# Kernel optimization log

Measured on AMD Instinct MI355X. Metric: run time of the kernel, lower is better.

## Reference

```python
import math
import jax, jax.numpy as jnp
import numpy as np

B, S, D = 8, 1024, 1024
H, DK = 16, 64
NUM_BUCKETS, MAX_DIST = 32, 128


def _relative_position_bucket(relative_position, num_buckets=NUM_BUCKETS, max_distance=MAX_DIST):
    # bidirectional=True branch of T5's bucket fn
    nb = num_buckets // 2
    n = -relative_position
    ret = (n < 0).astype(jnp.int32) * nb
    n = jnp.abs(n)
    max_exact = nb // 2
    is_small = n < max_exact
    n_safe = jnp.maximum(n, 1).astype(jnp.float32)
    val_if_large = max_exact + (
        jnp.log(n_safe / max_exact) / math.log(max_distance / max_exact) * (nb - max_exact)
    ).astype(jnp.int32)
    val_if_large = jnp.minimum(val_if_large, nb - 1)
    return ret + jnp.where(is_small, n, val_if_large)


def compute_bias(rel_emb, qlen, klen):
    ctx = jnp.arange(qlen)[:, None]
    mem = jnp.arange(klen)[None, :]
    rp_bucket = _relative_position_bucket(mem - ctx)          # [q, k]
    values = rel_emb[rp_bucket]                                # [q, k, H]
    return jnp.transpose(values, (2, 0, 1))[None]              # [1, H, q, k]


def setup_inputs() -> dict:
    key = jax.random.key(0)
    ks = jax.random.split(key, 6)
    sc = 0.02
    return {
        "x": jax.random.normal(ks[0], (B, S, D), jnp.float32),
        "Wq": jax.random.normal(ks[1], (D, H * DK), jnp.float32) * sc,
        "Wk": jax.random.normal(ks[2], (D, H * DK), jnp.float32) * sc,
        "Wv": jax.random.normal(ks[3], (D, H * DK), jnp.float32) * sc,
        "Wo": jax.random.normal(ks[4], (H * DK, D), jnp.float32) * sc,
        "rel_emb": jax.random.normal(ks[5], (NUM_BUCKETS, H), jnp.float32),
    }


def reference(x, Wq, Wk, Wv, Wo, rel_emb):
    bs, qlen, _ = x.shape

    def shape(t):  # [B, S, H*DK] -> [B, H, S, DK]
        return t.reshape(bs, -1, H, DK).transpose(0, 2, 1, 3)

    q = shape(x @ Wq)
    k = shape(x @ Wk)
    v = shape(x @ Wv)
    # T5 attention: NO 1/sqrt(dk) scaling
    scores = jnp.einsum("bhqd,bhkd->bhqk", q, k)
    position_bias = compute_bias(rel_emb, qlen, qlen)
    scores = scores + position_bias
    weights = jax.nn.softmax(scores.astype(jnp.float32), axis=-1).astype(scores.dtype)
    context = jnp.einsum("bhqk,bhkd->bhqd", weights, v)
    context = context.transpose(0, 2, 1, 3).reshape(bs, qlen, H * DK)
    return context @ Wo
```

## Files before the change

kernel.cpp:

```cpp
#include <hip/hip_runtime.h>
#include <stdint.h>

typedef uint16_t u16;
typedef uint32_t u32;
typedef __bf16 bf16;
typedef bf16 bf16x8 __attribute__((ext_vector_type(8)));
typedef bf16 bf16x4 __attribute__((ext_vector_type(4)));
typedef float f32x4 __attribute__((ext_vector_type(4)));
typedef u16 u16x4 __attribute__((ext_vector_type(4)));

#define MFMA(a, b, c) __builtin_amdgcn_mfma_f32_16x16x32_bf16((a), (b), (c), 0, 0, 0)

#define BATCH 8
#define SEQ 1024
#define DMODEL 1024
#define NH 16
#define DK 64
#define LOG2E 1.4426950408889634f

__device__ __forceinline__ u16 bfbits(float f) {
    bf16 h = (bf16)f;
    return __builtin_bit_cast(u16, h);
}

__device__ __forceinline__ float exp2_raw(float x) {
    float r;
    asm("v_exp_f32 %0, %1" : "=v"(r) : "v"(x));
    return r;
}

__device__ __forceinline__ void gload_lds16(const u16* g, u16* l) {
    __builtin_amdgcn_global_load_lds(
        (__attribute__((address_space(1))) void*)g,
        (__attribute__((address_space(3))) void*)l, 16, 0, 0);
}

__global__ __launch_bounds__(256) void prep_kernel(
        const float* __restrict__ x, const float* __restrict__ W0,
        const float* __restrict__ W1, const float* __restrict__ W2,
        const float* __restrict__ W3, const float* __restrict__ rel_emb,
        u16* __restrict__ xb, u16* __restrict__ T0, u16* __restrict__ T1,
        u16* __restrict__ T2, u16* __restrict__ T3, f32x4* __restrict__ F4) {
    __shared__ u16 Ts[64 * 72];
    const int bid = blockIdx.x, tid = threadIdx.x;
    if (bid < 8192) {
        size_t id = (size_t)bid * 256 + tid;
        f32x4 v = *(const f32x4*)(x + id * 4);
        bf16x4 o;
        o[0] = (bf16)v[0]; o[1] = (bf16)v[1]; o[2] = (bf16)v[2]; o[3] = (bf16)v[3];
        *(bf16x4*)(xb + id * 4) = o;
    } else if (bid < 9216) {
        const int t = bid - 8192;
        const int z = t >> 8, rem = t & 255;
        const float* W = (z == 0) ? W0 : (z == 1) ? W1 : (z == 2) ? W2 : W3;
        u16* T = (z == 0) ? T0 : (z == 1) ? T1 : (z == 2) ? T2 : T3;
        const int k0 = (rem >> 4) * 64, n0 = (rem & 15) * 64;
        const int r16 = tid >> 4, c0 = (tid & 15) * 4;
        #pragma unroll
        for (int rr = 0; rr < 4; rr++) {
            int r = rr * 16 + r16;
            f32x4 vv = *(const f32x4*)&W[(size_t)(k0 + r) * 1024 + n0 + c0];
            #pragma unroll
            for (int i = 0; i < 4; i++) Ts[(c0 + i) * 72 + r] = bfbits(vv[i]);
        }
        __syncthreads();
        int n = tid >> 2, seg = (tid & 3) * 16;
        *(bf16x8*)&T[(size_t)(n0 + n) * 1024 + k0 + seg] = *(const bf16x8*)&Ts[n * 72 + seg];
        *(bf16x8*)&T[(size_t)(n0 + n) * 1024 + k0 + seg + 8] =
            *(const bf16x8*)&Ts[n * 72 + seg + 8];
    } else {
        int id = (bid - 9216) * 256 + tid;
        if (id >= NH * 2047) return;
        int h = id / 2047, tt0 = id % 2047;
        f32x4 o;
        #pragma unroll
        for (int j = 0; j < 4; j++) {
            int tt = tt0 + j;
            float val = 0.f;
            if (tt <= 2046) {
                int rel = tt - 1023;
                int n = -rel;
                int b = 0;
                if (n < 0) { b = 16; n = -n; }
                int v;
                if (n < 8) {
                    v = n;
                } else {
                    int e = 31 - __clz(n);
                    int f = 2 * e + ((unsigned)(n * n) >= (1u << (2 * e + 1)) ? 1 : 0);
                    v = min(2 + f, 15);
                }
                val = LOG2E * rel_emb[(b + v) * NH + h];
            }
            o[j] = val;
        }
        F4[(size_t)h * 2047 + tt0] = o;
    }
}

__global__ __launch_bounds__(256) void gemm_qkv_kernel(
        const u16* __restrict__ xb,
        const u16* __restrict__ Wqt, const u16* __restrict__ Wkt, const u16* __restrict__ Wvt,
        u16* __restrict__ qb, u16* __restrict__ kb, u16* __restrict__ vb) {
    __shared__ u16 As[8192];
    __shared__ u16 Bs[8192];
    const int z = blockIdx.y >> 3;
    const u16* Bt = (z == 0) ? Wqt : (z == 1) ? Wkt : Wvt;
    const int m0 = blockIdx.x * 128, n0 = (blockIdx.y & 7) * 128;
    const int tid = threadIdx.x, w = tid >> 6, lane = tid & 63;
    const int quad = lane >> 4, l16 = lane & 15;
    const int rw = w >> 1, cw = w & 1;
    const int srow = lane >> 2, sseg = lane & 3;

    f32x4 acc[4][4];
    #pragma unroll
    for (int i = 0; i < 4; i++)
        #pragma unroll
        for (int j = 0; j < 4; j++) acc[i][j] = (f32x4){0.f, 0.f, 0.f, 0.f};

    for (int kk = 0; kk < 1024; kk += 64) {
        __syncthreads();
        #pragma unroll
        for (int p = 0; p < 2; p++) {
            #pragma unroll
            for (int r = 0; r < 2; r++) {
                int base = r * 64 + w * 16;
                int row = base + srow;
                gload_lds16(&xb[(size_t)(m0 + row) * 1024 + kk + p * 32 + sseg * 8],
                            &As[p * 4096 + base * 32]);
                gload_lds16(&Bt[(size_t)(n0 + row) * 1024 + kk + p * 32 + sseg * 8],
                            &Bs[p * 4096 + base * 32]);
            }
        }
        __syncthreads();
        #pragma unroll
        for (int p = 0; p < 2; p++) {
            bf16x8 af[4], bfr[4];
            #pragma unroll
            for (int mt = 0; mt < 4; mt++)
                af[mt] = *(const bf16x8*)&As[p * 4096 + (rw * 64 + mt * 16 + l16) * 32 + quad * 8];
            #pragma unroll
            for (int nt = 0; nt < 4; nt++)
                bfr[nt] = *(const bf16x8*)&Bs[p * 4096 + (cw * 64 + nt * 16 + l16) * 32 + quad * 8];
            #pragma unroll
            for (int mt = 0; mt < 4; mt++)
                #pragma unroll
                for (int nt = 0; nt < 4; nt++)
                    acc[mt][nt] = MFMA(af[mt], bfr[nt], acc[mt][nt]);
        }
    }

    #pragma unroll
    for (int mt = 0; mt < 4; mt++) {
        int gmBase = m0 + rw * 64 + mt * 16 + quad * 4;
        #pragma unroll
        for (int nt = 0; nt < 4; nt++) {
            int gn = n0 + cw * 64 + nt * 16 + l16;
            int h = gn >> 6, dk = gn & 63;
            if (z == 2) {
                int b_ = gmBase >> 10, s0 = gmBase & 1023;
                u16x4 pk = { bfbits(acc[mt][nt][0]), bfbits(acc[mt][nt][1]),
                             bfbits(acc[mt][nt][2]), bfbits(acc[mt][nt][3]) };
                *(u16x4*)&vb[(((size_t)b_ * NH + h) * DK + dk) * SEQ + s0] = pk;
            } else {
                u16* o = z ? kb : qb;
                #pragma unroll
                for (int r = 0; r < 4; r++) {
                    int gm = gmBase + r;
                    int b_ = gm >> 10, s = gm & 1023;
                    float sv = acc[mt][nt][r];
                    if (z == 0) sv *= LOG2E;
                    o[(((size_t)b_ * NH + h) * SEQ + s) * DK + dk] = bfbits(sv);
                }
            }
        }
    }
}

__global__ __launch_bounds__(256) void gemm_out_kernel(
        const u16* __restrict__ ctx, const u16* __restrict__ Wot, float* __restrict__ out) {
    __shared__ u16 As[8192];
    __shared__ u16 Bs[8192];
    const int m0 = blockIdx.x * 128, n0 = blockIdx.y * 128;
    const int tid = threadIdx.x, w = tid >> 6, lane = tid & 63;
    const int quad = lane >> 4, l16 = lane & 15;
    const int rw = w >> 1, cw = w & 1;
    const int srow = lane >> 2, sseg = lane & 3;

    f32x4 acc[4][4];
    #pragma unroll
    for (int i = 0; i < 4; i++)
        #pragma unroll
        for (int j = 0; j < 4; j++) acc[i][j] = (f32x4){0.f, 0.f, 0.f, 0.f};

    for (int kk = 0; kk < 1024; kk += 64) {
        __syncthreads();
        #pragma unroll
        for (int p = 0; p < 2; p++) {
            #pragma unroll
            for (int r = 0; r < 2; r++) {
                int base = r * 64 + w * 16;
                int row = base + srow;
                gload_lds16(&ctx[(size_t)(m0 + row) * 1024 + kk + p * 32 + sseg * 8],
                            &As[p * 4096 + base * 32]);
                gload_lds16(&Wot[(size_t)(n0 + row) * 1024 + kk + p * 32 + sseg * 8],
                            &Bs[p * 4096 + base * 32]);
            }
        }
        __syncthreads();
        #pragma unroll
        for (int p = 0; p < 2; p++) {
            bf16x8 af[4], bfr[4];
            #pragma unroll
            for (int mt = 0; mt < 4; mt++)
                af[mt] = *(const bf16x8*)&As[p * 4096 + (rw * 64 + mt * 16 + l16) * 32 + quad * 8];
            #pragma unroll
            for (int nt = 0; nt < 4; nt++)
                bfr[nt] = *(const bf16x8*)&Bs[p * 4096 + (cw * 64 + nt * 16 + l16) * 32 + quad * 8];
            #pragma unroll
            for (int mt = 0; mt < 4; mt++)
                #pragma unroll
                for (int nt = 0; nt < 4; nt++)
                    acc[mt][nt] = MFMA(af[mt], bfr[nt], acc[mt][nt]);
        }
    }

    #pragma unroll
    for (int mt = 0; mt < 4; mt++) {
        int gmBase = m0 + rw * 64 + mt * 16 + quad * 4;
        #pragma unroll
        for (int nt = 0; nt < 4; nt++) {
            int gn = n0 + cw * 64 + nt * 16 + l16;
            #pragma unroll
            for (int r = 0; r < 4; r++)
                out[(size_t)(gmBase + r) * 1024 + gn] = acc[mt][nt][r];
        }
    }
}

__global__ __launch_bounds__(256) void attn_kernel(
        const u16* __restrict__ qb, const u16* __restrict__ kb,
        const u16* __restrict__ vb, const f32x4* __restrict__ F4,
        u16* __restrict__ ctx) {
    __shared__ u16 Kt[64 * 72];
    __shared__ u16 Vt[64 * 72];
    __shared__ u16 Pt[4][32 * 40];
    const int bh = blockIdx.x;
    const int h = bh & (NH - 1), b_ = bh >> 4;
    const int tid = threadIdx.x, w = tid >> 6, lane = tid & 63;
    const int quad = lane >> 4, l16 = lane & 15;
    const int q0 = blockIdx.y * 128 + w * 32;

    const f32x4* F4h = F4 + (size_t)h * 2047;

    bf16x8 bq[2][2];
    #pragma unroll
    for (int mt = 0; mt < 2; mt++) {
        const u16* qrow = qb + ((size_t)bh * SEQ + q0 + mt * 16 + l16) * DK;
        bq[mt][0] = *(const bf16x8*)(qrow + quad * 8);
        bq[mt][1] = *(const bf16x8*)(qrow + 32 + quad * 8);
    }

    float l_[2] = {0.f, 0.f};
    f32x4 oacc[2][4];
    #pragma unroll
    for (int mt = 0; mt < 2; mt++)
        #pragma unroll
        for (int dt = 0; dt < 4; dt++) oacc[mt][dt] = (f32x4){0.f, 0.f, 0.f, 0.f};

    const int srow = tid >> 3, sseg = tid & 7;

    const u16* kbase_p = kb + (size_t)bh * SEQ * DK;
    const u16* vbase_p = vb + (size_t)bh * DK * SEQ;

    bf16x8 kr0 = *(const bf16x8*)&kbase_p[(size_t)srow * DK + sseg * 8];
    bf16x8 kr1 = *(const bf16x8*)&kbase_p[(size_t)(srow + 32) * DK + sseg * 8];
    bf16x8 vr0 = *(const bf16x8*)&vbase_p[(size_t)srow * SEQ + sseg * 8];
    bf16x8 vr1 = *(const bf16x8*)&vbase_p[(size_t)(srow + 32) * SEQ + sseg * 8];

    for (int kt = 0; kt < 16; kt++) {
        const int kbase = kt * 64;
        __syncthreads();
        *(bf16x8*)&Kt[srow * 72 + sseg * 8] = kr0;
        *(bf16x8*)&Kt[(srow + 32) * 72 + sseg * 8] = kr1;
        *(bf16x8*)&Vt[srow * 72 + sseg * 8] = vr0;
        *(bf16x8*)&Vt[(srow + 32) * 72 + sseg * 8] = vr1;
        if (kt < 15) {
            const int nb = kbase + 64;
            kr0 = *(const bf16x8*)&kbase_p[(size_t)(nb + srow) * DK + sseg * 8];
            kr1 = *(const bf16x8*)&kbase_p[(size_t)(nb + srow + 32) * DK + sseg * 8];
            vr0 = *(const bf16x8*)&vbase_p[(size_t)srow * SEQ + nb + sseg * 8];
            vr1 = *(const bf16x8*)&vbase_p[(size_t)(srow + 32) * SEQ + nb + sseg * 8];
        }
        __syncthreads();

        f32x4 sc[2][4];
        #pragma unroll
        for (int mt = 0; mt < 2; mt++)
            #pragma unroll
            for (int nt = 0; nt < 4; nt++) {
                int t0 = (kbase + nt * 16 + quad * 4) - (q0 + mt * 16 + l16) + 1023;
                sc[mt][nt] = F4h[t0];
            }
        #pragma unroll
        for (int nt = 0; nt < 4; nt++) {
            bf16x8 ak0 = *(const bf16x8*)&Kt[(nt * 16 + l16) * 72 + quad * 8];
            bf16x8 ak1 = *(const bf16x8*)&Kt[(nt * 16 + l16) * 72 + 32 + quad * 8];
            #pragma unroll
            for (int mt = 0; mt < 2; mt++) {
                sc[mt][nt] = MFMA(ak0, bq[mt][0], sc[mt][nt]);
                sc[mt][nt] = MFMA(ak1, bq[mt][1], sc[mt][nt]);
            }
        }

        #pragma unroll
        for (int c = 0; c < 2; c++) {
            #pragma unroll
            for (int mt = 0; mt < 2; mt++) {
                #pragma unroll
                for (int i = 0; i < 2; i++) {
                    int nt = 2 * c + i;
                    float p0 = exp2_raw(sc[mt][nt][0]);
                    float p1 = exp2_raw(sc[mt][nt][1]);
                    float p2 = exp2_raw(sc[mt][nt][2]);
                    float p3 = exp2_raw(sc[mt][nt][3]);
                    l_[mt] += (p0 + p1) + (p2 + p3);
                    bf16x4 pk;
                    pk[0] = (bf16)p0; pk[1] = (bf16)p1;
                    pk[2] = (bf16)p2; pk[3] = (bf16)p3;
                    *(bf16x4*)&Pt[w][(mt * 16 + l16) * 40 + i * 16 + quad * 4] = pk;
                }
            }
            bf16x8 bp[2];
            #pragma unroll
            for (int mt = 0; mt < 2; mt++)
                bp[mt] = *(const bf16x8*)&Pt[w][(mt * 16 + l16) * 40 + quad * 8];
            #pragma unroll
            for (int dt = 0; dt < 4; dt++) {
                bf16x8 av = *(const bf16x8*)&Vt[(dt * 16 + l16) * 72 + c * 32 + quad * 8];
                #pragma unroll
                for (int mt = 0; mt < 2; mt++)
                    oacc[mt][dt] = MFMA(av, bp[mt], oacc[mt][dt]);
            }
        }
    }

    #pragma unroll
    for (int mt = 0; mt < 2; mt++) {
        float l = l_[mt];
        l += __shfl_xor(l, 16, 64);
        l += __shfl_xor(l, 32, 64);
        float inv = 1.f / l;
        int gq = q0 + mt * 16 + l16;
        #pragma unroll
        for (int dt = 0; dt < 4; dt++) {
            u16x4 pk = { bfbits(oacc[mt][dt][0] * inv), bfbits(oacc[mt][dt][1] * inv),
                         bfbits(oacc[mt][dt][2] * inv), bfbits(oacc[mt][dt][3] * inv) };
            *(u16x4*)&ctx[((size_t)b_ * SEQ + gq) * DMODEL + h * DK + dt * 16 + quad * 4] = pk;
        }
    }
}

extern "C" void kernel_launch(void* const* d_in, const int* in_sizes, int n_in,
                              void* d_out, int out_size, void* d_ws, size_t ws_size,
                              hipStream_t stream) {
    const float* x   = (const float*)d_in[0];
    const float* Wq  = (const float*)d_in[1];
    const float* Wk  = (const float*)d_in[2];
    const float* Wv  = (const float*)d_in[3];
    const float* Wo  = (const float*)d_in[4];
    const float* rel = (const float*)d_in[5];
    float* out = (float*)d_out;

    char* p = (char*)d_ws;
    u16* xb  = (u16*)p; p += (size_t)BATCH * SEQ * DMODEL * 2;
    u16* Wqt = (u16*)p; p += (size_t)DMODEL * DMODEL * 2;
    u16* Wkt = (u16*)p; p += (size_t)DMODEL * DMODEL * 2;
    u16* Wvt = (u16*)p; p += (size_t)DMODEL * DMODEL * 2;
    u16* Wot = (u16*)p; p += (size_t)DMODEL * DMODEL * 2;
    u16* qb  = (u16*)p; p += (size_t)BATCH * NH * SEQ * DK * 2;
    u16* kb  = (u16*)p; p += (size_t)BATCH * NH * SEQ * DK * 2;
    u16* vb  = (u16*)p; p += (size_t)BATCH * NH * SEQ * DK * 2;
    u16* ctx = (u16*)p; p += (size_t)BATCH * SEQ * DMODEL * 2;
    f32x4* F4 = (f32x4*)p; p += (size_t)NH * 2047 * 16;

    prep_kernel<<<9344, 256, 0, stream>>>(x, Wq, Wk, Wv, Wo, rel,
                                          xb, Wqt, Wkt, Wvt, Wot, F4);

    gemm_qkv_kernel<<<dim3(64, 24), 256, 0, stream>>>(xb, Wqt, Wkt, Wvt, qb, kb, vb);

    attn_kernel<<<dim3(128, 8), 256, 0, stream>>>(qb, kb, vb, F4, ctx);

    gemm_out_kernel<<<dim3(64, 8), 256, 0, stream>>>(ctx, Wot, out);
}
```

Measured before the change: 250.0 us.

## Rewrite QKV GEMM as 256x256 tile 8-wave pipelined kernel with swizzled LDS

Replaces the 128x128, 4-wave QKV projection GEMM with a 256x256 tile, 8-wave kernel. Global-to-LDS loads are double-buffered in half-tiles and interleaved with MFMA phases using explicit waitcnt, barriers, sched_barrier and setprio. LDS rows use an XOR swizzle to avoid bank conflicts. The aim is to hide load latency and raise data reuse per tile, at the cost of 64KB LDS per block, a much more complex schedule, and fewer blocks (384) across the device.

```diff
diff --git a/kernel.cpp b/kernel.cpp
--- a/kernel.cpp
+++ b/kernel.cpp
@@ -98,64 +98,106 @@
     }
 }
 
-__global__ __launch_bounds__(256) void gemm_qkv_kernel(
+__device__ __forceinline__ void stage_half(const u16* __restrict__ g, u16* l,
+                                           int wid, int lane) {
+    const int rl = lane >> 3, slot = lane & 7;
+    const int seg = (slot ^ rl) * 8;
+    const int r0 = wid * 8 + rl;
+    gload_lds16(&g[(size_t)r0 * 1024 + seg],        l + wid * 512);
+    gload_lds16(&g[(size_t)(r0 + 64) * 1024 + seg], l + 4096 + wid * 512);
+}
+
+__global__ __launch_bounds__(512, 2) void gemm_qkv8_kernel(
         const u16* __restrict__ xb,
         const u16* __restrict__ Wqt, const u16* __restrict__ Wkt, const u16* __restrict__ Wvt,
         u16* __restrict__ qb, u16* __restrict__ kb, u16* __restrict__ vb) {
-    __shared__ u16 As[8192];
-    __shared__ u16 Bs[8192];
-    const int z = blockIdx.y >> 3;
+    __shared__ u16 lds[2][2][2][8192];
+    const int z = blockIdx.y >> 2;
     const u16* Bt = (z == 0) ? Wqt : (z == 1) ? Wkt : Wvt;
-    const int m0 = blockIdx.x * 128, n0 = (blockIdx.y & 7) * 128;
-    const int tid = threadIdx.x, w = tid >> 6, lane = tid & 63;
+    const int m0 = blockIdx.x * 256, n0 = (blockIdx.y & 3) * 256;
+    const int tid = threadIdx.x, wid = tid >> 6, lane = tid & 63;
     const int quad = lane >> 4, l16 = lane & 15;
-    const int rw = w >> 1, cw = w & 1;
-    const int srow = lane >> 2, sseg = lane & 3;
-
-    f32x4 acc[4][4];
-    #pragma unroll
-    for (int i = 0; i < 4; i++)
+    const int wr = wid >> 2, wc = wid & 3;
+    const int swz = l16 & 7;
+
+    const u16* Abase = xb + (size_t)m0 * 1024;
+    const u16* Bbase = Bt + (size_t)n0 * 1024;
+
+    f32x4 acc[8][4];
+    #pragma unroll
+    for (int i = 0; i < 8; i++)
         #pragma unroll
         for (int j = 0; j < 4; j++) acc[i][j] = (f32x4){0.f, 0.f, 0.f, 0.f};
-
-    for (int kk = 0; kk < 1024; kk += 64) {
-        __syncthreads();
-        #pragma unroll
-        for (int p = 0; p < 2; p++) {
-            #pragma unroll
-            for (int r = 0; r < 2; r++) {
-                int base = r * 64 + w * 16;
-                int row = base + srow;
-                gload_lds16(&xb[(size_t)(m0 + row) * 1024 + kk + p * 32 + sseg * 8],
-                            &As[p * 4096 + base * 32]);
-                gload_lds16(&Bt[(size_t)(n0 + row) * 1024 + kk + p * 32 + sseg * 8],
-                            &Bs[p * 4096 + base * 32]);
-            }
-        }
-        __syncthreads();
-        #pragma unroll
-        for (int p = 0; p < 2; p++) {
-            bf16x8 af[4], bfr[4];
-            #pragma unroll
-            for (int mt = 0; mt < 4; mt++)
-                af[mt] = *(const bf16x8*)&As[p * 4096 + (rw * 64 + mt * 16 + l16) * 32 + quad * 8];
-            #pragma unroll
-            for (int nt = 0; nt < 4; nt++)
-                bfr[nt] = *(const bf16x8*)&Bs[p * 4096 + (cw * 64 + nt * 16 + l16) * 32 + quad * 8];
-            #pragma unroll
-            for (int mt = 0; mt < 4; mt++)
+    bf16x8 bfrag[4][2];
+
+    stage_half(Bbase,                   &lds[0][1][0][0], wid, lane);
+    stage_half(Bbase + 128 * 1024,      &lds[0][1][1][0], wid, lane);
+    stage_half(Abase,                   &lds[0][0][0][0], wid, lane);
+    stage_half(Abase + 128 * 1024,      &lds[0][0][1][0], wid, lane);
+    stage_half(Bbase + 64,              &lds[1][1][0][0], wid, lane);
+    stage_half(Bbase + 128 * 1024 + 64, &lds[1][1][1][0], wid, lane);
+    stage_half(Abase + 64,              &lds[1][0][0][0], wid, lane);
+    asm volatile("s_waitcnt vmcnt(6)" ::: "memory");
+    __builtin_amdgcn_s_barrier();
+
+    #pragma unroll 1
+    for (int t = 0; t < 8; t++) {
+        #pragma unroll
+        for (int ph = 0; ph < 8; ph++) {
+            const int bb = ph >> 2, q = ph & 3;
+            bf16x8 a_[2][2];
+            const u16* Ah = &lds[bb][0][q >> 1][0];
+            #pragma unroll
+            for (int mh = 0; mh < 2; mh++) {
+                int row = (wr << 6) + (((2 * q + mh) & 3) << 4) + l16;
+                #pragma unroll
+                for (int kk = 0; kk < 2; kk++)
+                    a_[mh][kk] = *(const bf16x8*)&Ah[row * 64 + ((((kk << 2) | quad) ^ swz) << 3)];
+            }
+            if (q == 0) {
+                const u16* Bh = &lds[bb][1][wc >> 1][0];
+                #pragma unroll
+                for (int nt = 0; nt < 4; nt++) {
+                    int row = ((wc & 1) << 6) + (nt << 4) + l16;
+                    #pragma unroll
+                    for (int kk = 0; kk < 2; kk++)
+                        bfrag[nt][kk] = *(const bf16x8*)&Bh[row * 64 + ((((kk << 2) | quad) ^ swz) << 3)];
+                }
+            }
+            {
+                const int sAB   = (ph == 0 || ph == 3 || ph == 4 || ph == 7) ? 0 : 1;
+                const int sbuf  = (ph >= 1 && ph <= 4) ? 0 : 1;
+                const int shalf = (ph & 1) ? 0 : 1;
+                int stile = (ph == 0) ? (2 * t + 1) : ((ph <= 4) ? (2 * t + 2) : (2 * t + 3));
+                stile = stile < 15 ? stile : 15;
+                const u16* src = (sAB ? Bbase : Abase) + (size_t)(shalf * 128) * 1024 + stile * 64;
+                stage_half(src, &lds[sbuf][sAB][shalf][0], wid, lane);
+            }
+            if (q == 0) asm volatile("s_waitcnt lgkmcnt(8)" ::: "memory");
+            __builtin_amdgcn_s_barrier();
+            asm volatile("s_waitcnt lgkmcnt(0)" ::: "memory");
+            __builtin_amdgcn_sched_barrier(0);
+            __builtin_amdgcn_s_setprio(1);
+            #pragma unroll
+            for (int mh = 0; mh < 2; mh++)
                 #pragma unroll
                 for (int nt = 0; nt < 4; nt++)
-                    acc[mt][nt] = MFMA(af[mt], bfr[nt], acc[mt][nt]);
-        }
-    }
-
-    #pragma unroll
-    for (int mt = 0; mt < 4; mt++) {
-        int gmBase = m0 + rw * 64 + mt * 16 + quad * 4;
+                    #pragma unroll
+                    for (int kk = 0; kk < 2; kk++)
+                        acc[2 * q + mh][nt] = MFMA(a_[mh][kk], bfrag[nt][kk], acc[2 * q + mh][nt]);
+            __builtin_amdgcn_s_setprio(0);
+            __builtin_amdgcn_sched_barrier(0);
+            if (q == 3) asm volatile("s_waitcnt vmcnt(6)" ::: "memory");
+            __builtin_amdgcn_s_barrier();
+        }
+    }
+
+    #pragma unroll
+    for (int mt = 0; mt < 8; mt++) {
+        int gmBase = m0 + ((mt >> 2) << 7) + (wr << 6) + ((mt & 3) << 4) + (quad << 2);
         #pragma unroll
         for (int nt = 0; nt < 4; nt++) {
-            int gn = n0 + cw * 64 + nt * 16 + l16;
+            int gn = n0 + (wc << 6) + (nt << 4) + l16;
             int h = gn >> 6, dk = gn & 63;
             if (z == 2) {
                 int b_ = gmBase >> 10, s0 = gmBase & 1023;
@@ -387,7 +429,7 @@
     prep_kernel<<<9344, 256, 0, stream>>>(x, Wq, Wk, Wv, Wo, rel,
                                           xb, Wqt, Wkt, Wvt, Wot, F4);
 
-    gemm_qkv_kernel<<<dim3(64, 24), 256, 0, stream>>>(xb, Wqt, Wkt, Wvt, qb, kb, vb);
+    gemm_qkv8_kernel<<<dim3(32, 12), 512, 0, stream>>>(xb, Wqt, Wkt, Wvt, qb, kb, vb);
 
     attn_kernel<<<dim3(128, 8), 256, 0, stream>>>(qb, kb, vb, F4, ctx);
 
```

Result: no change. 245.3 us (-1.9%).
